# Optimization experiments

Hardware: AMD Instinct MI355X
Metric: run time of the kernel (lower is better)

Reference implementation:

```python
import jax, jax.numpy as jnp
import numpy as np

REG_PARAM = 0.05  # entropic regularisation (> 0 -> logsumexp branch)
N, M, D = 8192, 16384, 64


def setup_inputs() -> dict:
    key = jax.random.key(0)
    k1, k2 = jax.random.split(key)
    source_data = jax.random.normal(k1, (N, D), dtype=jnp.float32)
    target_data = jax.random.normal(k2, (M, D), dtype=jnp.float32)
    psi = jnp.zeros((M,), dtype=jnp.float32)
    return {"source_data": source_data, "target_data": target_data, "psi": psi}


def reference(source_data, target_data, psi):
    reg = jnp.float32(REG_PARAM)
    m = target_data.shape[0]
    # squared norms of target atoms, shape [M]; normalization = their mean
    sq_target = jnp.sum(target_data * target_data, axis=1)
    cost_norm = jnp.mean(sq_target)
    # pairwise squared distances [N, M], normalized
    sq_source = jnp.sum(source_data * source_data, axis=1, keepdims=True)  # [N,1]
    cross = jnp.matmul(source_data, target_data.T)                         # [N,M]
    cost_matrix = (sq_source + sq_target[None, :] - 2.0 * cross) / cost_norm
    # entropic semi-dual: mean(-reg * logsumexp((psi - C)/reg + log nu)) + mean(psi)
    log_nu = -jnp.log(jnp.float32(m))  # nu = uniform 1/M
    lse = jax.nn.logsumexp((psi[None, :] - cost_matrix) / reg + log_nu, axis=1)  # [N]
    return jnp.mean(-reg * lse) + jnp.mean(psi)
```

## Files before the change

kernel.cpp:

```cpp
#include <hip/hip_runtime.h>
#include <math.h>
#include <stdint.h>

#define N_SRC 8192
#define M_TGT 16384
#define DDIM  64
#define REG_P 0.05f
#define LOG2E 1.44269504088896340736f
#define LN2   0.69314718055994530942f
#define QSPLIT 8

typedef __attribute__((ext_vector_type(8))) short short8;
typedef __attribute__((ext_vector_type(4))) float f32x4;

#define OFF_TGT  0u
#define OFF_SRC  (2u << 20)
#define OFF_SQT  (3u << 20)
#define OFF_SQS  ((3u << 20) + 65536u)
#define OFF_PART ((3u << 20) + 98304u)
#define OFF_L    ((3u << 20) + 102400u)

#define K1_BLOCKS 384

__device__ __forceinline__ unsigned short f2bf(float f) {
    unsigned u = __float_as_uint(f);
    u += 0x7fffu + ((u >> 16) & 1u);
    return (unsigned short)(u >> 16);
}

__device__ __forceinline__ float fast_exp2(float x) {
#if __has_builtin(__builtin_amdgcn_exp2f)
    return __builtin_amdgcn_exp2f(x);
#else
    return exp2f(x);
#endif
}

__global__ __launch_bounds__(256) void k1_stage(const float* __restrict__ src,
                                                const float* __restrict__ tgt,
                                                const float* __restrict__ psi,
                                                char* __restrict__ ws) {
    const int tid  = threadIdx.x;
    const int wave = tid >> 6;
    const int lane = tid & 63;
    const int lo   = lane & 15;
    const int hi   = lane >> 4;
    const int task = blockIdx.x * 4 + wave;

    float sq_contrib = 0.f;
    float ps_contrib = 0.f;

    if (task < 1024) {
        const int T = task;
        const int j = T * 16 + lo;
        float sq = 0.f;
#pragma unroll
        for (int kk = 0; kk < 2; ++kk) {
            const float* p = tgt + (size_t)j * DDIM + kk * 32 + hi * 8;
            float4 v0 = ((const float4*)p)[0];
            float4 v1 = ((const float4*)p)[1];
            short8 pk;
            pk[0]=(short)f2bf(v0.x); pk[1]=(short)f2bf(v0.y); pk[2]=(short)f2bf(v0.z); pk[3]=(short)f2bf(v0.w);
            pk[4]=(short)f2bf(v1.x); pk[5]=(short)f2bf(v1.y); pk[6]=(short)f2bf(v1.z); pk[7]=(short)f2bf(v1.w);
            ((short8*)(ws + OFF_TGT))[(T * 2 + kk) * 64 + lane] = pk;
            sq += v0.x*v0.x + v0.y*v0.y + v0.z*v0.z + v0.w*v0.w
                + v1.x*v1.x + v1.y*v1.y + v1.z*v1.z + v1.w*v1.w;
        }
        float r = sq;
        r += __shfl_xor(r, 16); r += __shfl_xor(r, 32);
        if (hi == 0) {
            ((float*)(ws + OFF_SQT))[j] = r;
            ps_contrib = psi[j];
        }
        sq_contrib = sq;
    } else {
        const int g = task - 1024;
        const int i = g * 16 + lo;
        float sq = 0.f;
#pragma unroll
        for (int kk = 0; kk < 2; ++kk) {
            const float* p = src + (size_t)i * DDIM + kk * 32 + hi * 8;
            float4 v0 = ((const float4*)p)[0];
            float4 v1 = ((const float4*)p)[1];
            short8 pk;
            pk[0]=(short)f2bf(v0.x); pk[1]=(short)f2bf(v0.y); pk[2]=(short)f2bf(v0.z); pk[3]=(short)f2bf(v0.w);
            pk[4]=(short)f2bf(v1.x); pk[5]=(short)f2bf(v1.y); pk[6]=(short)f2bf(v1.z); pk[7]=(short)f2bf(v1.w);
            ((short8*)(ws + OFF_SRC))[(g * 2 + kk) * 64 + lane] = pk;
            sq += v0.x*v0.x + v0.y*v0.y + v0.z*v0.z + v0.w*v0.w
                + v1.x*v1.x + v1.y*v1.y + v1.z*v1.z + v1.w*v1.w;
        }
        float r = sq;
        r += __shfl_xor(r, 16); r += __shfl_xor(r, 32);
        if (hi == 0) ((float*)(ws + OFF_SQS))[i] = r;
    }

    float a = sq_contrib, b = ps_contrib;
#pragma unroll
    for (int off = 1; off < 64; off <<= 1) {
        a += __shfl_xor(a, off);
        b += __shfl_xor(b, off);
    }
    __shared__ float s_a[4], s_b[4];
    if (lane == 0) { s_a[wave] = a; s_b[wave] = b; }
    __syncthreads();
    if (tid == 0) {
        float2 out;
        out.x = s_a[0] + s_a[1] + s_a[2] + s_a[3];
        out.y = s_b[0] + s_b[1] + s_b[2] + s_b[3];
        ((float2*)(ws + OFF_PART))[blockIdx.x] = out;
    }
}

__global__ __launch_bounds__(256, 4) void k2_main(const float* __restrict__ psi,
                                                  char* __restrict__ ws) {
    const int tid    = threadIdx.x;
    const int lane   = tid & 63;
    const int w      = tid >> 6;
    const int rowblk = blockIdx.x >> 3;
    const int q      = blockIdx.x & (QSPLIT - 1);
    const int row0   = rowblk * 64;

    const float2* __restrict__ part = (const float2*)(ws + OFF_PART);
    float ssq = 0.f;
#pragma unroll
    for (int k = 0; k < K1_BLOCKS / 64; ++k) ssq += part[k * 64 + lane].x;
#pragma unroll
    for (int off = 1; off < 64; off <<= 1) ssq += __shfl_xor(ssq, off);
    const float inv_cn = (float)M_TGT / ssq;
    const float c_psi  = (1.0f / REG_P) * LOG2E;
    const float c_sqt  = inv_cn * c_psi;
    const float alpha2 = 2.0f * c_sqt;

    const short8* __restrict__ srcst = (const short8*)(ws + OFF_SRC);
    short8 Af[4][2];
#pragma unroll
    for (int g = 0; g < 4; ++g)
#pragma unroll
        for (int kk = 0; kk < 2; ++kk)
            Af[g][kk] = srcst[((row0 >> 4) + g) * 128 + kk * 64 + lane];

    const short8* __restrict__ tgtst = (const short8*)(ws + OFF_TGT);
    const float*  __restrict__ sqt   = (const float*)(ws + OFF_SQT);

    const int T0    = (q * 2048 + w * 512) >> 4;
    const int jlane = (T0 << 4) + (lane & 15);

    float lsum[4][4];
#pragma unroll
    for (int g = 0; g < 4; ++g)
#pragma unroll
        for (int r = 0; r < 4; ++r) lsum[g][r] = 0.f;

    short8 B0n = tgtst[(T0 * 2 + 0) * 64 + lane];
    short8 B1n = tgtst[(T0 * 2 + 1) * 64 + lane];
    float  psn = psi[jlane];
    float  sqn = sqt[jlane];

    for (int t = 0; t < 32; ++t) {
        short8 B0 = B0n, B1 = B1n;
        float  ps = psn, sq = sqn;
        if (t < 31) {
            const int Tg = T0 + t + 1;
            B0n = tgtst[(Tg * 2 + 0) * 64 + lane];
            B1n = tgtst[(Tg * 2 + 1) * 64 + lane];
            psn = psi[jlane + (t + 1) * 16];
            sqn = sqt[jlane + (t + 1) * 16];
        }
        const float bias = ps * c_psi - sq * c_sqt;
        f32x4 acc[4];
#pragma unroll
        for (int g = 0; g < 4; ++g) {
            f32x4 a = {0.f, 0.f, 0.f, 0.f};
            a = __builtin_amdgcn_mfma_f32_16x16x32_bf16(Af[g][0], B0, a, 0, 0, 0);
            a = __builtin_amdgcn_mfma_f32_16x16x32_bf16(Af[g][1], B1, a, 0, 0, 0);
            acc[g] = a;
        }
#pragma unroll
        for (int g = 0; g < 4; ++g)
#pragma unroll
            for (int r = 0; r < 4; ++r)
                lsum[g][r] += fast_exp2(fmaf(alpha2, acc[g][r], bias));
    }

    __shared__ float s_l[4][64];
#pragma unroll
    for (int g = 0; g < 4; ++g)
#pragma unroll
        for (int r = 0; r < 4; ++r) {
            float v = lsum[g][r];
            v += __shfl_xor(v, 1); v += __shfl_xor(v, 2);
            v += __shfl_xor(v, 4); v += __shfl_xor(v, 8);
            if ((lane & 15) == 0)
                s_l[w][g * 16 + (lane >> 4) * 4 + r] = v;
        }
    __syncthreads();
    if (tid < 64) {
        float v = s_l[0][tid] + s_l[1][tid] + s_l[2][tid] + s_l[3][tid];
        ((float*)(ws + OFF_L))[q * N_SRC + row0 + tid] = v;
    }
}

__global__ __launch_bounds__(1024) void k3_final(const char* __restrict__ ws,
                                                 float* __restrict__ out) {
    const int tid  = threadIdx.x;
    const int lane = tid & 63;

    const float2* __restrict__ part = (const float2*)(ws + OFF_PART);
    float ssq = 0.f, spsi = 0.f;
#pragma unroll
    for (int k = 0; k < K1_BLOCKS / 64; ++k) {
        float2 p = part[k * 64 + lane];
        ssq += p.x; spsi += p.y;
    }
#pragma unroll
    for (int off = 1; off < 64; off <<= 1) {
        ssq  += __shfl_xor(ssq, off);
        spsi += __shfl_xor(spsi, off);
    }
    const float inv_cn = (float)M_TGT / ssq;

    const float* __restrict__ L   = (const float*)(ws + OFF_L);
    const float* __restrict__ sqs = (const float*)(ws + OFF_SQS);
    const float logM = logf((float)M_TGT);

    float acc = 0.f;
    for (int i = tid; i < N_SRC; i += 1024) {
        float lt = 0.f;
#pragma unroll
        for (int qq = 0; qq < QSPLIT; ++qq) lt += L[qq * N_SRC + i];
        const float A = -sqs[i] * inv_cn * (1.0f / REG_P) - logM;
        acc += -REG_P * (A + LN2 * __log2f(lt));
    }
    __shared__ float red[1024];
    red[tid] = acc;
    __syncthreads();
    for (int off = 512; off > 0; off >>= 1) {
        if (tid < off) red[tid] += red[tid + off];
        __syncthreads();
    }
    if (tid == 0)
        out[0] = red[0] / (float)N_SRC + spsi / (float)M_TGT;
}

extern "C" void kernel_launch(void* const* d_in, const int* in_sizes, int n_in,
                              void* d_out, int out_size, void* d_ws, size_t ws_size,
                              hipStream_t stream) {
    const float* src = (const float*)d_in[0];
    const float* tgt = (const float*)d_in[1];
    const float* psi = (const float*)d_in[2];
    char* ws = (char*)d_ws;

    k1_stage<<<K1_BLOCKS, 256, 0, stream>>>(src, tgt, psi, ws);
    k2_main<<<(N_SRC / 64) * QSPLIT, 256, 0, stream>>>(psi, ws);
    k3_final<<<1, 1024, 0, stream>>>(ws, (float*)d_out);
}
```

Before: 100.5 us.

## Fuse final reduction into main kernel via atomic last-block counters

Removes the separate single-block k3_final launch. The last of the QSPLIT column-split blocks for each row block now computes that block's log terms, and the last row block adds up the partials and writes the output, coordinated through agent-scope atomic counters that k1 zeroes. It also packs psi*c and the squared target norms into one float2 array so each tile needs a single bias load instead of two. This saves a kernel launch and a serial 1024-thread tail in exchange for atomics and a counter reset protocol.

```diff
diff --git a/kernel.cpp b/kernel.cpp
--- a/kernel.cpp
+++ b/kernel.cpp
@@ -8,17 +8,21 @@
 #define REG_P 0.05f
 #define LOG2E 1.44269504088896340736f
 #define LN2   0.69314718055994530942f
+#define LOGM  9.70406052783923404f
 #define QSPLIT 8
+#define NROWBLK (N_SRC / 64)
 
 typedef __attribute__((ext_vector_type(8))) short short8;
 typedef __attribute__((ext_vector_type(4))) float f32x4;
 
 #define OFF_TGT  0u
 #define OFF_SRC  (2u << 20)
-#define OFF_SQT  (3u << 20)
-#define OFF_SQS  ((3u << 20) + 65536u)
-#define OFF_PART ((3u << 20) + 98304u)
-#define OFF_L    ((3u << 20) + 102400u)
+#define OFF_BT   (3u << 20)
+#define OFF_SQS  ((3u << 20) + (128u << 10))
+#define OFF_PART ((3u << 20) + (160u << 10))
+#define OFF_CNT  ((3u << 20) + (164u << 10))
+#define OFF_RBP  ((3u << 20) + (166u << 10))
+#define OFF_L    ((3u << 20) + (168u << 10))
 
 #define K1_BLOCKS 384
 
@@ -47,6 +51,11 @@
     const int hi   = lane >> 4;
     const int task = blockIdx.x * 4 + wave;
 
+    if (blockIdx.x == 0 && tid < 129)
+        ((unsigned*)(ws + OFF_CNT))[tid] = 0u;
+
+    const float c_psi = (1.0f / REG_P) * LOG2E;
+
     float sq_contrib = 0.f;
     float ps_contrib = 0.f;
 
@@ -69,8 +78,9 @@
         float r = sq;
         r += __shfl_xor(r, 16); r += __shfl_xor(r, 32);
         if (hi == 0) {
-            ((float*)(ws + OFF_SQT))[j] = r;
-            ps_contrib = psi[j];
+            float pv = psi[j];
+            ((float2*)(ws + OFF_BT))[j] = make_float2(pv * c_psi, r);
+            ps_contrib = pv;
         }
         sq_contrib = sq;
     } else {
@@ -111,8 +121,8 @@
     }
 }
 
-__global__ __launch_bounds__(256, 4) void k2_main(const float* __restrict__ psi,
-                                                  char* __restrict__ ws) {
+__global__ __launch_bounds__(256, 4) void k2_main(char* __restrict__ ws,
+                                                  float* __restrict__ out) {
     const int tid    = threadIdx.x;
     const int lane   = tid & 63;
     const int w      = tid >> 6;
@@ -121,11 +131,17 @@
     const int row0   = rowblk * 64;
 
     const float2* __restrict__ part = (const float2*)(ws + OFF_PART);
-    float ssq = 0.f;
-#pragma unroll
-    for (int k = 0; k < K1_BLOCKS / 64; ++k) ssq += part[k * 64 + lane].x;
-#pragma unroll
-    for (int off = 1; off < 64; off <<= 1) ssq += __shfl_xor(ssq, off);
+    float ssq = 0.f, spsi = 0.f;
+#pragma unroll
+    for (int k = 0; k < K1_BLOCKS / 64; ++k) {
+        float2 p = part[k * 64 + lane];
+        ssq += p.x; spsi += p.y;
+    }
+#pragma unroll
+    for (int off = 1; off < 64; off <<= 1) {
+        ssq  += __shfl_xor(ssq, off);
+        spsi += __shfl_xor(spsi, off);
+    }
     const float inv_cn = (float)M_TGT / ssq;
     const float c_psi  = (1.0f / REG_P) * LOG2E;
     const float c_sqt  = inv_cn * c_psi;
@@ -140,7 +156,7 @@
             Af[g][kk] = srcst[((row0 >> 4) + g) * 128 + kk * 64 + lane];
 
     const short8* __restrict__ tgtst = (const short8*)(ws + OFF_TGT);
-    const float*  __restrict__ sqt   = (const float*)(ws + OFF_SQT);
+    const float2* __restrict__ btp   = (const float2*)(ws + OFF_BT);
 
     const int T0    = (q * 2048 + w * 512) >> 4;
     const int jlane = (T0 << 4) + (lane & 15);
@@ -153,20 +169,18 @@
 
     short8 B0n = tgtst[(T0 * 2 + 0) * 64 + lane];
     short8 B1n = tgtst[(T0 * 2 + 1) * 64 + lane];
-    float  psn = psi[jlane];
-    float  sqn = sqt[jlane];
+    float2 btn = btp[jlane];
 
     for (int t = 0; t < 32; ++t) {
         short8 B0 = B0n, B1 = B1n;
-        float  ps = psn, sq = sqn;
+        float2 bt = btn;
         if (t < 31) {
             const int Tg = T0 + t + 1;
             B0n = tgtst[(Tg * 2 + 0) * 64 + lane];
             B1n = tgtst[(Tg * 2 + 1) * 64 + lane];
-            psn = psi[jlane + (t + 1) * 16];
-            sqn = sqt[jlane + (t + 1) * 16];
-        }
-        const float bias = ps * c_psi - sq * c_sqt;
+            btn = btp[jlane + (t + 1) * 16];
+        }
+        const float bias = fmaf(-c_sqt, bt.y, bt.x);
         f32x4 acc[4];
 #pragma unroll
         for (int g = 0; g < 4; ++g) {
@@ -194,52 +208,59 @@
                 s_l[w][g * 16 + (lane >> 4) * 4 + r] = v;
         }
     __syncthreads();
+
     if (tid < 64) {
         float v = s_l[0][tid] + s_l[1][tid] + s_l[2][tid] + s_l[3][tid];
         ((float*)(ws + OFF_L))[q * N_SRC + row0 + tid] = v;
-    }
-}
-
-__global__ __launch_bounds__(1024) void k3_final(const char* __restrict__ ws,
-                                                 float* __restrict__ out) {
-    const int tid  = threadIdx.x;
-    const int lane = tid & 63;
-
-    const float2* __restrict__ part = (const float2*)(ws + OFF_PART);
-    float ssq = 0.f, spsi = 0.f;
-#pragma unroll
-    for (int k = 0; k < K1_BLOCKS / 64; ++k) {
-        float2 p = part[k * 64 + lane];
-        ssq += p.x; spsi += p.y;
-    }
-#pragma unroll
-    for (int off = 1; off < 64; off <<= 1) {
-        ssq  += __shfl_xor(ssq, off);
-        spsi += __shfl_xor(spsi, off);
-    }
-    const float inv_cn = (float)M_TGT / ssq;
-
-    const float* __restrict__ L   = (const float*)(ws + OFF_L);
-    const float* __restrict__ sqs = (const float*)(ws + OFF_SQS);
-    const float logM = logf((float)M_TGT);
-
-    float acc = 0.f;
-    for (int i = tid; i < N_SRC; i += 1024) {
-        float lt = 0.f;
-#pragma unroll
-        for (int qq = 0; qq < QSPLIT; ++qq) lt += L[qq * N_SRC + i];
-        const float A = -sqs[i] * inv_cn * (1.0f / REG_P) - logM;
-        acc += -REG_P * (A + LN2 * __log2f(lt));
-    }
-    __shared__ float red[1024];
-    red[tid] = acc;
-    __syncthreads();
-    for (int off = 512; off > 0; off >>= 1) {
-        if (tid < off) red[tid] += red[tid + off];
-        __syncthreads();
-    }
-    if (tid == 0)
-        out[0] = red[0] / (float)N_SRC + spsi / (float)M_TGT;
+
+        unsigned* cnt = (unsigned*)(ws + OFF_CNT);
+        int lastf = 0;
+        if (lane == 0) {
+            unsigned old = __hip_atomic_fetch_add(cnt + rowblk, 1u,
+                                                  __ATOMIC_ACQ_REL,
+                                                  __HIP_MEMORY_SCOPE_AGENT);
+            lastf = (old == QSPLIT - 1) ? 1 : 0;
+        }
+        lastf = __shfl(lastf, 0);
+
+        if (lastf) {
+            __threadfence();
+            const float* __restrict__ L   = (const float*)(ws + OFF_L);
+            const float* __restrict__ sqs = (const float*)(ws + OFF_SQS);
+            const int i = row0 + lane;
+            float lt = 0.f;
+#pragma unroll
+            for (int qq = 0; qq < QSPLIT; ++qq) lt += L[qq * N_SRC + i];
+            const float A = -sqs[i] * inv_cn * (1.0f / REG_P) - LOGM;
+            float c = -REG_P * (A + LN2 * __log2f(lt));
+#pragma unroll
+            for (int off = 1; off < 64; off <<= 1) c += __shfl_xor(c, off);
+
+            int fin = 0;
+            if (lane == 0) {
+                ((float*)(ws + OFF_RBP))[rowblk] = c;
+                unsigned old2 = __hip_atomic_fetch_add(cnt + 128, 1u,
+                                                       __ATOMIC_ACQ_REL,
+                                                       __HIP_MEMORY_SCOPE_AGENT);
+                fin = (old2 == NROWBLK - 1) ? 1 : 0;
+            }
+            fin = __shfl(fin, 0);
+
+            if (fin) {
+                __threadfence();
+                const float* __restrict__ rbp = (const float*)(ws + OFF_RBP);
+                float tsum = rbp[lane] + rbp[lane + 64];
+#pragma unroll
+                for (int off = 1; off < 64; off <<= 1) tsum += __shfl_xor(tsum, off);
+                if (lane == 0)
+                    out[0] = tsum / (float)N_SRC + spsi / (float)M_TGT;
+
+                cnt[lane] = 0u;
+                cnt[lane + 64] = 0u;
+                if (lane == 0) cnt[128] = 0u;
+            }
+        }
+    }
 }
 
 extern "C" void kernel_launch(void* const* d_in, const int* in_sizes, int n_in,
@@ -251,6 +272,5 @@
     char* ws = (char*)d_ws;
 
     k1_stage<<<K1_BLOCKS, 256, 0, stream>>>(src, tgt, psi, ws);
-    k2_main<<<(N_SRC / 64) * QSPLIT, 256, 0, stream>>>(psi, ws);
-    k3_final<<<1, 1024, 0, stream>>>(ws, (float*)d_out);
-}
+    k2_main<<<NROWBLK * QSPLIT, 256, 0, stream>>>(ws, (float*)d_out);
+}
```

Measured after the change: 126.9 us. +26.3%, slower.
